# Performance work log

Measured on AMD Instinct MI355X. Metric: run time of the kernel, lower is better.

Reference implementation:

```python
import jax, jax.numpy as jnp
import numpy as np

N, E, G = 50000, 600000, 64
MUL = 16        # hidden multiplicity: 16x0e + 16x1o -> node feature dim 16 + 48 = 64
MIN_ = 8        # input multiplicity: 8x0e + 8x1o -> input dim 8 + 24 = 32
NUM_LAYERS = 3
INV_S3 = float(1.0 / np.sqrt(3.0))   # CG norm for 1o x 1o -> 0e (dot)
INV_S2 = float(1.0 / np.sqrt(2.0))   # CG norm for 1o x 1o -> 1o (cross)
NORM_S = float(1.0 / np.sqrt(2 * MUL * MUL))  # fan-in: two paths feed 0e output
NORM_V = float(1.0 / np.sqrt(3 * MUL * MUL))  # fan-in: three paths feed 1o output
INV_LIN_IN = float(1.0 / np.sqrt(MIN_))
INV_LIN_OUT = float(1.0 / np.sqrt(MUL))


def _pair(a, b, W):
    # a: [E,u], b: [E,v], W: [u,v,w] -> [E,w]; opt_einsum keeps intermediates at E*MUL^2
    return jnp.einsum('eu,ev,uvw->ew', a, b, W)


def _tp(s1, v1, s2, v2, W):
    """FullyConnectedTensorProduct for (16x0e+16x1o) x (16x0e+16x1o) -> (16x0e+16x1o).
    s*: [E,MUL] scalars, v*: [E,MUL,3] vectors, W: [5,MUL,MUL,MUL] per-path weights."""
    # 0e outputs: 0e*0e->0e  and  1o.1o->0e (dot product, CG = delta/sqrt(3))
    p1 = _pair(s1, s2, W[0])
    p4 = sum(_pair(v1[:, :, i], v2[:, :, i], W[3]) for i in range(3))
    out_s = (p1 + p4 * INV_S3) * NORM_S
    # 1o outputs: 0e*1o->1o, 1o*0e->1o, 1o x 1o -> 1o (cross, CG = eps/sqrt(2))
    p2 = jnp.einsum('eu,evi,uvw->ewi', s1, v2, W[1])
    p3 = jnp.einsum('eui,ev,uvw->ewi', v1, s2, W[2])
    cyc = [(1, 2), (2, 0), (0, 1)]  # eps_ijk: out_k = a_i b_j - a_j b_i
    p5 = jnp.stack([_pair(v1[:, :, i], v2[:, :, j], W[4]) - _pair(v1[:, :, j], v2[:, :, i], W[4])
                    for (i, j) in cyc], axis=-1)
    out_v = (p2 + p3 + p5 * INV_S2) * NORM_V
    return out_s, out_v


def _gate(s, v):
    # irreps-aware Gate: scalars through SiLU, vectors gated by sigmoid of matching scalars
    return jax.nn.silu(s), v * jax.nn.sigmoid(s)[:, :, None]


def setup_inputs() -> dict:
    key = jax.random.key(0)
    ks = jax.random.split(key, 8)
    x = jax.random.normal(ks[0], (N, MIN_ + 3 * MIN_), dtype=jnp.float32)
    row = jax.random.randint(ks[1], (E,), 0, N, dtype=jnp.int32)
    col = jax.random.randint(ks[2], (E,), 0, N, dtype=jnp.int32)
    batch_idx = jnp.sort(jax.random.randint(ks[3], (N,), 0, G, dtype=jnp.int32))
    w_in0 = jax.random.normal(ks[4], (MIN_, MUL), dtype=jnp.float32)   # input Linear 0e->0e
    w_in1 = jax.random.normal(ks[5], (MIN_, MUL), dtype=jnp.float32)   # input Linear 1o->1o
    tp_w = jax.random.normal(ks[6], (NUM_LAYERS, 5, MUL, MUL, MUL), dtype=jnp.float32)
    w_out0 = jax.random.normal(ks[7], (MUL, 1), dtype=jnp.float32)     # readout Linear 0e->0e
    return dict(x=x, row=row, col=col, batch_idx=batch_idx,
                w_in0=w_in0, w_in1=w_in1, tp_w=tp_w, w_out0=w_out0)


def reference(x, row, col, batch_idx, w_in0, w_in1, tp_w, w_out0):
    n = x.shape[0]
    # irreps Linear input projection (per-irrep multiplicity mixing, e3nn-normalized)
    s = (x[:, :MIN_] @ w_in0) * INV_LIN_IN                                  # [N,MUL]
    v = jnp.einsum('nui,uw->nwi', x[:, MIN_:].reshape(n, MIN_, 3), w_in1) * INV_LIN_IN  # [N,MUL,3]
    for l in range(NUM_LAYERS):
        ms, mv = _tp(s[row], v[row], s[col], v[col], tp_w[l])  # gather + CG tensor product
        s = jax.ops.segment_sum(ms, row, num_segments=n)       # scatter-add to destination
        v = jax.ops.segment_sum(mv, row, num_segments=n)
        s, v = _gate(s, v)
    node_out = (s @ w_out0)[:, 0] * INV_LIN_OUT                # readout Linear -> 1x0e
    energy = jax.ops.segment_sum(node_out, batch_idx, num_segments=G)  # per-graph energy
    return energy
```

## Files before the change

### kernel.cpp

```cpp
#include <hip/hip_runtime.h>

#define N_NODES 50000
#define N_EDGES 600000
#define N_GRAPHS 64
#define N_TILES (N_EDGES / 16)
#define NPART 196
#define EDGE_GRID 1536

#define INV_LIN_IN  0.35355339059327373f
#define INV_LIN_OUT 0.25f
#define C_INV_S3    0.5773502691896258f
#define C_INV_S2    0.7071067811865476f
#define C_NORM_S    0.04419417382415922f
#define C_NORM_V    0.036084391824351615f

#define ALPHA      0.03125f
#define W_UNSCALE  1024.0f

typedef __attribute__((ext_vector_type(8))) _Float16 h16x8;
typedef __attribute__((ext_vector_type(4))) _Float16 h16x4;
typedef __attribute__((ext_vector_type(2))) _Float16 h16x2;
typedef __attribute__((ext_vector_type(4))) float f32x4;

__global__ void hist_kernel(const int* __restrict__ row, int* __restrict__ counts) {
    int e = blockIdx.x * 256 + threadIdx.x;
    if (e < N_EDGES) atomicAdd(&counts[row[e]], 1);
}

__global__ void scan_part_kernel(const int* __restrict__ counts, int* __restrict__ partial) {
    __shared__ int sm[256];
    int t = threadIdx.x;
    int i = blockIdx.x * 256 + t;
    sm[t] = (i < N_NODES) ? counts[i] : 0;
    __syncthreads();
    for (int s = 128; s > 0; s >>= 1) {
        if (t < s) sm[t] += sm[t + s];
        __syncthreads();
    }
    if (t == 0) partial[blockIdx.x] = sm[0];
}

__global__ void scan_partials_kernel(const int* __restrict__ partial, int* __restrict__ partOff) {
    __shared__ int sm[256];
    int t = threadIdx.x;
    int v = (t < NPART) ? partial[t] : 0;
    sm[t] = v;
    __syncthreads();
    for (int s = 1; s < 256; s <<= 1) {
        int add = (t >= s) ? sm[t - s] : 0;
        __syncthreads();
        sm[t] += add;
        __syncthreads();
    }
    if (t < NPART) partOff[t] = sm[t] - v;
}

__global__ void scan_final_kernel(const int* __restrict__ counts,
                                  const int* __restrict__ partOff,
                                  int* __restrict__ cursor) {
    __shared__ int sm[256];
    int t = threadIdx.x;
    int i = blockIdx.x * 256 + t;
    int v = (i < N_NODES) ? counts[i] : 0;
    sm[t] = v;
    __syncthreads();
    for (int s = 1; s < 256; s <<= 1) {
        int add = (t >= s) ? sm[t - s] : 0;
        __syncthreads();
        sm[t] += add;
        __syncthreads();
    }
    if (i < N_NODES) cursor[i] = sm[t] - v + partOff[blockIdx.x];
}

__global__ void scatter_kernel(const int* __restrict__ row, const int* __restrict__ col,
                               int* __restrict__ cursor, int* __restrict__ sortedRC) {
    int e = blockIdx.x * 256 + threadIdx.x;
    if (e < N_EDGES) {
        int n = row[e];
        int pos = atomicAdd(&cursor[n], 1);
        sortedRC[pos] = n | (col[e] << 16);
    }
}

__global__ void init_kernel(const float* __restrict__ x,
                            const float* __restrict__ w_in0,
                            const float* __restrict__ w_in1,
                            const float* __restrict__ tp_w,
                            h16x4* __restrict__ featH,
                            _Float16* __restrict__ wh,
                            int* __restrict__ counts,
                            float* __restrict__ energy) {
    int gid = blockIdx.x * 256 + threadIdx.x;

    if (gid < 64) energy[gid] = 0.f;
    if (gid < N_NODES) counts[gid] = 0;

    if (gid < 3 * 20480) {
        int i = gid;
        int j    = i & 7;
        int t1   = i >> 3;
        int lane = t1 & 63;
        int t2   = t1 >> 6;
        int c    = t2 & 7;
        int t3   = t2 >> 3;
        int slot = t3 % 5;
        int l    = t3 / 5;
        int p = (slot == 0) ? 1 : (slot == 1) ? 2 : (slot == 2) ? 4 : (slot == 3) ? 0 : 3;
        int kk = c * 32 + (lane >> 4) * 8 + j;
        int u = kk >> 4, v = kk & 15, n = lane & 15;
        float scale;
        if      (p == 0) scale = C_NORM_S;
        else if (p == 3) scale = C_INV_S3 * C_NORM_S;
        else if (p == 4) scale = C_INV_S2 * C_NORM_V;
        else             scale = C_NORM_V;
        if (l > 0) scale *= W_UNSCALE;
        float val = tp_w[(size_t)(l * 5 + p) * 4096 + u * 256 + v * 16 + n] * scale;
        wh[i] = (_Float16)val;
    }

    if (gid < N_NODES) {
        const float* xp = x + (size_t)gid * 32;
        float xs[8], xvx[8], xvy[8], xvz[8];
#pragma unroll
        for (int u = 0; u < 8; ++u) xs[u] = xp[u];
#pragma unroll
        for (int u = 0; u < 8; ++u) {
            xvx[u] = xp[8 + 3 * u + 0];
            xvy[u] = xp[8 + 3 * u + 1];
            xvz[u] = xp[8 + 3 * u + 2];
        }
#pragma unroll
        for (int w = 0; w < 16; ++w) {
            float s = 0.f, vx = 0.f, vy = 0.f, vz = 0.f;
#pragma unroll
            for (int u = 0; u < 8; ++u) {
                float a0 = w_in0[u * 16 + w];
                float a1 = w_in1[u * 16 + w];
                s  += xs[u]  * a0;
                vx += xvx[u] * a1;
                vy += xvy[u] * a1;
                vz += xvz[u] * a1;
            }
            h16x4 o;
            o.x = (_Float16)(s  * INV_LIN_IN);
            o.y = (_Float16)(vx * INV_LIN_IN);
            o.z = (_Float16)(vy * INV_LIN_IN);
            o.w = (_Float16)(vz * INV_LIN_IN);
            featH[(size_t)gid * 16 + w] = o;
        }
    }
}

__global__ __launch_bounds__(256, 4)
void edge_tp_kernel(const h16x4* __restrict__ feat,
                    float* __restrict__ out,
                    const int* __restrict__ sortedRC,
                    const _Float16* __restrict__ wh) {
    __shared__ h16x8 sW[1536];

    const int t = threadIdx.x;
    {
        const int4* src = (const int4*)wh;
        int4* dst = (int4*)sW;
#pragma unroll
        for (int i = 0; i < 6; ++i) dst[t + 256 * i] = src[t + 256 * i];
    }
    __syncthreads();

    const int lane = t & 63;
    const int wave = t >> 6;
    const int q = lane >> 4;
    const int m = lane & 15;
    const int v0 = (q & 1) * 8;

    const h16x8* gw = ((const h16x8*)wh) + 1536;

    const int gw_id = blockIdx.x * 4 + wave;
    const int nw = gridDim.x * 4;
    int tile = (int)(((long long)gw_id * N_TILES) / nw);
    const int tileEnd = (int)(((long long)(gw_id + 1) * N_TILES) / nw);
    if (tile >= tileEnd) return;

    int rc = sortedRC[tile * 16 + m];
    h16x4 Bt[8];
    {
        const h16x4* bp = feat + (size_t)(((unsigned)rc) >> 16) * 16 + v0;
#pragma unroll
        for (int k = 0; k < 8; ++k) Bt[k] = bp[k];
    }

    for (; tile < tileEnd; ++tile) {
        const int myR = rc & 0xFFFF;
        const int nt = tile + 1;
        const int nrc = (nt < tileEnd) ? sortedRC[nt * 16 + m] : rc;

        h16x2 Bs[4], Bx[4], By[4], Bz[4];
#pragma unroll
        for (int k = 0; k < 4; ++k) {
            Bs[k].x = Bt[2 * k].x; Bs[k].y = Bt[2 * k + 1].x;
            Bx[k].x = Bt[2 * k].y; Bx[k].y = Bt[2 * k + 1].y;
            By[k].x = Bt[2 * k].z; By[k].y = Bt[2 * k + 1].z;
            Bz[k].x = Bt[2 * k].w; Bz[k].y = Bt[2 * k + 1].w;
        }

        f32x4 acc_s = {0.f, 0.f, 0.f, 0.f};
        f32x4 acc_x = {0.f, 0.f, 0.f, 0.f};
        f32x4 acc_y = {0.f, 0.f, 0.f, 0.f};
        f32x4 acc_z = {0.f, 0.f, 0.f, 0.f};

        const h16x4* ap = feat + (size_t)myR * 16;

#pragma unroll 4
        for (int c = 0; c < 8; ++c) {
            h16x8 w0f = gw[(0 * 8 + c) * 64 + lane];
            h16x8 w3f = gw[(1 * 8 + c) * 64 + lane];
            h16x8 w1f = sW[(0 * 8 + c) * 64 + lane];
            h16x8 w2f = sW[(1 * 8 + c) * 64 + lane];
            h16x8 w4f = sW[(2 * 8 + c) * 64 + lane];

            h16x4 A = ap[2 * c + (q >> 1)];
            h16x2 s2; s2.x = A.x; s2.y = A.x;
            h16x2 x2; x2.x = A.y; x2.y = A.y;
            h16x2 y2; y2.x = A.z; y2.y = A.z;
            h16x2 z2; z2.x = A.w; z2.y = A.w;

            union { h16x8 v; h16x2 h[4]; } z;

#pragma unroll
            for (int k = 0; k < 4; ++k) z.h[k] = s2 * Bs[k];
            acc_s = __builtin_amdgcn_mfma_f32_16x16x32_f16(z.v, w0f, acc_s, 0, 0, 0);

#pragma unroll
            for (int k = 0; k < 4; ++k)
                z.h[k] = x2 * Bx[k] + y2 * By[k] + z2 * Bz[k];
            acc_s = __builtin_amdgcn_mfma_f32_16x16x32_f16(z.v, w3f, acc_s, 0, 0, 0);

#pragma unroll
            for (int k = 0; k < 4; ++k) z.h[k] = s2 * Bx[k];
            acc_x = __builtin_amdgcn_mfma_f32_16x16x32_f16(z.v, w1f, acc_x, 0, 0, 0);
#pragma unroll
            for (int k = 0; k < 4; ++k) z.h[k] = x2 * Bs[k];
            acc_x = __builtin_amdgcn_mfma_f32_16x16x32_f16(z.v, w2f, acc_x, 0, 0, 0);
#pragma unroll
            for (int k = 0; k < 4; ++k) z.h[k] = y2 * Bz[k] - z2 * By[k];
            acc_x = __builtin_amdgcn_mfma_f32_16x16x32_f16(z.v, w4f, acc_x, 0, 0, 0);

#pragma unroll
            for (int k = 0; k < 4; ++k) z.h[k] = s2 * By[k];
            acc_y = __builtin_amdgcn_mfma_f32_16x16x32_f16(z.v, w1f, acc_y, 0, 0, 0);
#pragma unroll
            for (int k = 0; k < 4; ++k) z.h[k] = y2 * Bs[k];
            acc_y = __builtin_amdgcn_mfma_f32_16x16x32_f16(z.v, w2f, acc_y, 0, 0, 0);
#pragma unroll
            for (int k = 0; k < 4; ++k) z.h[k] = z2 * Bx[k] - x2 * Bz[k];
            acc_y = __builtin_amdgcn_mfma_f32_16x16x32_f16(z.v, w4f, acc_y, 0, 0, 0);

#pragma unroll
            for (int k = 0; k < 4; ++k) z.h[k] = s2 * Bz[k];
            acc_z = __builtin_amdgcn_mfma_f32_16x16x32_f16(z.v, w1f, acc_z, 0, 0, 0);
#pragma unroll
            for (int k = 0; k < 4; ++k) z.h[k] = z2 * Bs[k];
            acc_z = __builtin_amdgcn_mfma_f32_16x16x32_f16(z.v, w2f, acc_z, 0, 0, 0);
#pragma unroll
            for (int k = 0; k < 4; ++k) z.h[k] = x2 * By[k] - y2 * Bx[k];
            acc_z = __builtin_amdgcn_mfma_f32_16x16x32_f16(z.v, w4f, acc_z, 0, 0, 0);
        }

        {
            const h16x4* nbp = feat + (size_t)(((unsigned)nrc) >> 16) * 16 + v0;
#pragma unroll
            for (int k = 0; k < 8; ++k) Bt[k] = nbp[k];
        }

        int prevR = __shfl(myR, (lane + 63) & 63);
        int flag = (m == 0) || (myR != prevR);
        unsigned long long bal = __ballot(flag != 0);
        unsigned mask16 = (unsigned)(bal & 0xFFFFull);

        int nseg = __popc(mask16);
        unsigned rem = mask16;
        for (int s = 0; s < nseg; ++s) {
            int lo = __ffs(rem) - 1;
            rem &= rem - 1;
            int hi = rem ? (__ffs(rem) - 1) : 16;
            float ps = 0.f, px = 0.f, py = 0.f, pz = 0.f;
#pragma unroll
            for (int r = 0; r < 4; ++r) {
                int ei = q * 4 + r;
                bool in = (ei >= lo) && (ei < hi);
                ps += in ? acc_s[r] : 0.f;
                px += in ? acc_x[r] : 0.f;
                py += in ? acc_y[r] : 0.f;
                pz += in ? acc_z[r] : 0.f;
            }
            ps += __shfl_xor(ps, 16); ps += __shfl_xor(ps, 32);
            px += __shfl_xor(px, 16); px += __shfl_xor(px, 32);
            py += __shfl_xor(py, 16); py += __shfl_xor(py, 32);
            pz += __shfl_xor(pz, 16); pz += __shfl_xor(pz, 32);
            int node = __shfl(myR, lo);
            float val = (q == 0) ? ps : (q == 1) ? px : (q == 2) ? py : pz;
            atomicAdd(out + (size_t)node * 64 + m * 4 + q, val);
        }

        rc = nrc;
    }
}

__global__ void gate_half_kernel(float4* __restrict__ acc,
                                 h16x4* __restrict__ featH) {
    int i = blockIdx.x * 256 + threadIdx.x;
    if (i >= N_NODES * 16) return;
    float4 f = acc[i];
    float g = ALPHA / (1.f + __expf(-f.x));
    h16x4 o;
    o.x = (_Float16)(f.x * g);
    o.y = (_Float16)(f.y * g);
    o.z = (_Float16)(f.z * g);
    o.w = (_Float16)(f.w * g);
    featH[i] = o;
    acc[i] = make_float4(0.f, 0.f, 0.f, 0.f);
}

__global__ void gate_readout_kernel(const float4* __restrict__ feat,
                                    const int* __restrict__ batch_idx,
                                    const float* __restrict__ w_out,
                                    float* __restrict__ energy) {
    __shared__ float bins[N_GRAPHS];
    int t = threadIdx.x;
    if (t < N_GRAPHS) bins[t] = 0.f;
    __syncthreads();
    int n = blockIdx.x * 256 + t;
    if (n < N_NODES) {
        const float4* f = feat + (size_t)n * 16;
        float acc = 0.f;
#pragma unroll
        for (int w = 0; w < 16; ++w) {
            float s = f[w].x;
            float silu = s / (1.f + __expf(-s));
            acc += silu * w_out[w];
        }
        atomicAdd(&bins[batch_idx[n]], acc * INV_LIN_OUT);
    }
    __syncthreads();
    if (t < N_GRAPHS) atomicAdd(&energy[t], bins[t]);
}

extern "C" void kernel_launch(void* const* d_in, const int* in_sizes, int n_in,
                              void* d_out, int out_size, void* d_ws, size_t ws_size,
                              hipStream_t stream) {
    const float* x         = (const float*)d_in[0];
    const int*   row       = (const int*)d_in[1];
    const int*   col       = (const int*)d_in[2];
    const int*   batch_idx = (const int*)d_in[3];
    const float* w_in0     = (const float*)d_in[4];
    const float* w_in1     = (const float*)d_in[5];
    const float* tp_w      = (const float*)d_in[6];
    const float* w_out0    = (const float*)d_in[7];
    float* energy = (float*)d_out;

    float*    acc   = (float*)d_ws;
    _Float16* featA = (_Float16*)(acc + (size_t)N_NODES * 64);
    _Float16* featB = featA + (size_t)N_NODES * 64;
    _Float16* wh    = featB + (size_t)N_NODES * 64;
    int* sortedRC = (int*)(wh + 3 * 20480);
    int* counts  = (int*)acc;
    int* cursor  = counts + N_NODES;
    int* partial = cursor + N_NODES;
    int* partOff = partial + 256;

    init_kernel<<<(3 * 20480 + 255) / 256, 256, 0, stream>>>(
        x, w_in0, w_in1, tp_w, (h16x4*)featA, wh, counts, energy);

    hist_kernel<<<(N_EDGES + 255) / 256, 256, 0, stream>>>(row, counts);
    scan_part_kernel<<<NPART, 256, 0, stream>>>(counts, partial);
    scan_partials_kernel<<<1, 256, 0, stream>>>(partial, partOff);
    scan_final_kernel<<<NPART, 256, 0, stream>>>(counts, partOff, cursor);
    scatter_kernel<<<(N_EDGES + 255) / 256, 256, 0, stream>>>(row, col, cursor, sortedRC);

    hipMemsetAsync(acc, 0, (size_t)N_NODES * 64 * sizeof(float), stream);

    _Float16* fin = featA;
    _Float16* fnext = featB;
    for (int l = 0; l < 3; ++l) {
        edge_tp_kernel<<<EDGE_GRID, 256, 0, stream>>>(
            (const h16x4*)fin, acc, sortedRC, wh + (size_t)l * 20480);
        if (l < 2) {
            gate_half_kernel<<<(N_NODES * 16 + 255) / 256, 256, 0, stream>>>(
                (float4*)acc, (h16x4*)fnext);
            _Float16* tmp = fin; fin = fnext; fnext = tmp;
        } else {
            gate_readout_kernel<<<(N_NODES + 255) / 256, 256, 0, stream>>>(
                (const float4*)acc, batch_idx, w_out0, energy);
        }
    }
}
```

Measured before the change: 435.7 us.

## Raise edge kernel occupancy, merge scan kernels, fold accumulator memset into init

The edge tensor-product kernel now keeps only two of the five weight paths in shared memory and reads the W4 path from global/cache. This cuts LDS per block so the launch bound can go from 4 to 8 blocks per CU, and the grid grows from 1536 to 2048 blocks. The separate scan-of-partials kernel is folded into the final scan, where each block reduces its own prefix of the partial sums. The accumulator memset moves into the init kernel, and the counts buffer moves into featB so it no longer aliases acc. Together these aim to raise latency hiding and cut launch overhead, at the risk of register pressure or spills under the tighter launch bound and more global weight traffic.

```diff
diff --git a/kernel.cpp b/kernel.cpp
--- a/kernel.cpp
+++ b/kernel.cpp
@@ -5,7 +5,7 @@
 #define N_GRAPHS 64
 #define N_TILES (N_EDGES / 16)
 #define NPART 196
-#define EDGE_GRID 1536
+#define EDGE_GRID 2048
 
 #define INV_LIN_IN  0.35355339059327373f
 #define INV_LIN_OUT 0.25f
@@ -40,37 +40,29 @@
     if (t == 0) partial[blockIdx.x] = sm[0];
 }
 
-__global__ void scan_partials_kernel(const int* __restrict__ partial, int* __restrict__ partOff) {
+__global__ void scan_final_kernel(const int* __restrict__ counts,
+                                  const int* __restrict__ partial,
+                                  int* __restrict__ cursor) {
     __shared__ int sm[256];
+    __shared__ int sm2[256];
     int t = threadIdx.x;
-    int v = (t < NPART) ? partial[t] : 0;
+    int i = blockIdx.x * 256 + t;
+    int v = (i < N_NODES) ? counts[i] : 0;
     sm[t] = v;
-    __syncthreads();
+    sm2[t] = (t < NPART && t < blockIdx.x) ? partial[t] : 0;
+    __syncthreads();
+    for (int s = 128; s > 0; s >>= 1) {
+        if (t < s) sm2[t] += sm2[t + s];
+        __syncthreads();
+    }
+    int base = sm2[0];
     for (int s = 1; s < 256; s <<= 1) {
         int add = (t >= s) ? sm[t - s] : 0;
         __syncthreads();
         sm[t] += add;
         __syncthreads();
     }
-    if (t < NPART) partOff[t] = sm[t] - v;
-}
-
-__global__ void scan_final_kernel(const int* __restrict__ counts,
-                                  const int* __restrict__ partOff,
-                                  int* __restrict__ cursor) {
-    __shared__ int sm[256];
-    int t = threadIdx.x;
-    int i = blockIdx.x * 256 + t;
-    int v = (i < N_NODES) ? counts[i] : 0;
-    sm[t] = v;
-    __syncthreads();
-    for (int s = 1; s < 256; s <<= 1) {
-        int add = (t >= s) ? sm[t - s] : 0;
-        __syncthreads();
-        sm[t] += add;
-        __syncthreads();
-    }
-    if (i < N_NODES) cursor[i] = sm[t] - v + partOff[blockIdx.x];
+    if (i < N_NODES) cursor[i] = sm[t] - v + base;
 }
 
 __global__ void scatter_kernel(const int* __restrict__ row, const int* __restrict__ col,
@@ -90,11 +82,15 @@
                             h16x4* __restrict__ featH,
                             _Float16* __restrict__ wh,
                             int* __restrict__ counts,
-                            float* __restrict__ energy) {
+                            float* __restrict__ energy,
+                            float4* __restrict__ acc) {
     int gid = blockIdx.x * 256 + threadIdx.x;
 
     if (gid < 64) energy[gid] = 0.f;
     if (gid < N_NODES) counts[gid] = 0;
+
+    for (int idx = gid; idx < N_NODES * 16; idx += 61440)
+        acc[idx] = make_float4(0.f, 0.f, 0.f, 0.f);
 
     if (gid < 3 * 20480) {
         int i = gid;
@@ -152,19 +148,19 @@
     }
 }
 
-__global__ __launch_bounds__(256, 4)
+__global__ __launch_bounds__(256, 8)
 void edge_tp_kernel(const h16x4* __restrict__ feat,
                     float* __restrict__ out,
                     const int* __restrict__ sortedRC,
                     const _Float16* __restrict__ wh) {
-    __shared__ h16x8 sW[1536];
+    __shared__ h16x8 sW[1024];
 
     const int t = threadIdx.x;
     {
         const int4* src = (const int4*)wh;
         int4* dst = (int4*)sW;
 #pragma unroll
-        for (int i = 0; i < 6; ++i) dst[t + 256 * i] = src[t + 256 * i];
+        for (int i = 0; i < 4; ++i) dst[t + 256 * i] = src[t + 256 * i];
     }
     __syncthreads();
 
@@ -174,7 +170,7 @@
     const int m = lane & 15;
     const int v0 = (q & 1) * 8;
 
-    const h16x8* gw = ((const h16x8*)wh) + 1536;
+    const h16x8* gw = ((const h16x8*)wh) + 1024;
 
     const int gw_id = blockIdx.x * 4 + wave;
     const int nw = gridDim.x * 4;
@@ -213,11 +209,13 @@
 
 #pragma unroll 4
         for (int c = 0; c < 8; ++c) {
-            h16x8 w0f = gw[(0 * 8 + c) * 64 + lane];
-            h16x8 w3f = gw[(1 * 8 + c) * 64 + lane];
+            short w4s = 0;
+            h16x8 w4f = gw[(0 * 8 + c) * 64 + lane];
+            h16x8 w0f = gw[(1 * 8 + c) * 64 + lane];
+            h16x8 w3f = gw[(2 * 8 + c) * 64 + lane];
             h16x8 w1f = sW[(0 * 8 + c) * 64 + lane];
             h16x8 w2f = sW[(1 * 8 + c) * 64 + lane];
-            h16x8 w4f = sW[(2 * 8 + c) * 64 + lane];
+            (void)w4s;
 
             h16x4 A = ap[2 * c + (q >> 1)];
             h16x2 s2; s2.x = A.x; s2.y = A.x;
@@ -364,21 +362,17 @@
     _Float16* featB = featA + (size_t)N_NODES * 64;
     _Float16* wh    = featB + (size_t)N_NODES * 64;
     int* sortedRC = (int*)(wh + 3 * 20480);
-    int* counts  = (int*)acc;
+    int* counts  = (int*)featB;
     int* cursor  = counts + N_NODES;
     int* partial = cursor + N_NODES;
-    int* partOff = partial + 256;
 
     init_kernel<<<(3 * 20480 + 255) / 256, 256, 0, stream>>>(
-        x, w_in0, w_in1, tp_w, (h16x4*)featA, wh, counts, energy);
+        x, w_in0, w_in1, tp_w, (h16x4*)featA, wh, counts, energy, (float4*)acc);
 
     hist_kernel<<<(N_EDGES + 255) / 256, 256, 0, stream>>>(row, counts);
     scan_part_kernel<<<NPART, 256, 0, stream>>>(counts, partial);
-    scan_partials_kernel<<<1, 256, 0, stream>>>(partial, partOff);
-    scan_final_kernel<<<NPART, 256, 0, stream>>>(counts, partOff, cursor);
+    scan_final_kernel<<<NPART, 256, 0, stream>>>(counts, partial, cursor);
     scatter_kernel<<<(N_EDGES + 255) / 256, 256, 0, stream>>>(row, col, cursor, sortedRC);
-
-    hipMemsetAsync(acc, 0, (size_t)N_NODES * 64 * sizeof(float), stream);
 
     _Float16* fin = featA;
     _Float16* fnext = featB;
```

Result: slower. 482.7 us (+10.8%).
